# Performance work log

Measured on AMD Instinct MI355X. Metric: run time of the kernel, lower is better.

Reference implementation:

```python
import jax, jax.numpy as jnp
import numpy as np

TWO_PI = 2.0 * np.pi


def _unwrap(x):
    # torch: abs(x - 2*pi*round(x/(2*pi))) -> wrap to principal value, take magnitude
    return jnp.abs(x - TWO_PI * jnp.round(x / TWO_PI))


def _shift_diff_last(x):
    # Equivalent to matmul with M = triu(1,d=1)-triu(1,d=2)-eye (superdiag=+1, diag=-1):
    # out[..., 0] = -x[..., 0]; out[..., j] = x[..., j-1] - x[..., j]
    return jnp.concatenate([-x[..., :1], x[..., :-1] - x[..., 1:]], axis=-1)


def setup_inputs() -> dict:
    key = jax.random.key(0)
    k1, k2, k3, k4 = jax.random.split(key, 4)
    shape = (32, 1, 513, 512)  # [B, 1, nfreqs, frames]
    return {
        "spec_est_real": jax.random.normal(k1, shape, dtype=jnp.float32),
        "spec_est_imag": jax.random.normal(k2, shape, dtype=jnp.float32),
        "spec_ref_real": jax.random.normal(k3, shape, dtype=jnp.float32),
        "spec_ref_imag": jax.random.normal(k4, shape, dtype=jnp.float32),
    }


def reference(spec_est_real, spec_est_imag, spec_ref_real, spec_ref_imag):
    # torch.angle(complex).squeeze(1) -> [B, F, T]
    phase_g = jnp.arctan2(spec_est_imag, spec_est_real)[:, 0]
    phase_r = jnp.arctan2(spec_ref_imag, spec_ref_real)[:, 0]

    d = phase_r - phase_g  # [B, F, T]

    # IP loss
    ip_loss = jnp.mean(_unwrap(d))
    # GD: shift-difference along freq axis (GD_r - GD_g = shift_diff(phase_r - phase_g))
    gd_loss = jnp.mean(_unwrap(_shift_diff_last(jnp.swapaxes(d, 1, 2))))
    # PTD: shift-difference along time axis
    ptd_loss = jnp.mean(_unwrap(_shift_diff_last(d)))

    return ip_loss + gd_loss + ptd_loss
```

## Files before the change

kernel.cpp:

```cpp
#include <hip/hip_runtime.h>
#include <math.h>


#define NB 32
#define NF 513
#define NT 512
#define RPW 8
#define CHUNKS 65
#define NBLOCKS 520
#define NTOT 8404992LL

static __device__ __forceinline__ float fast_atan2(float y, float x) {
    const float PI_F  = 3.14159274101257324f;
    const float PI_2F = 1.57079632679489662f;
    float ax = fabsf(x), ay = fabsf(y);
    float mx = fmaxf(ax, ay), mn = fminf(ax, ay);
    float r  = mn * __builtin_amdgcn_rcpf(mx);
    r = (mx == 0.f) ? 0.f : r;
    float s = r * r;
    float p = fmaf(s, -0.01172120f, 0.05265332f);
    p = fmaf(s, p, -0.11643287f);
    p = fmaf(s, p,  0.19354346f);
    p = fmaf(s, p, -0.33262347f);
    p = fmaf(s, p,  0.99997726f);
    float a = r * p;
    a = (ay > ax) ? (PI_2F - a) : a;
    a = (x < 0.f) ? (PI_F - a) : a;
    return copysignf(a, y);
}

static __device__ __forceinline__ float pdiff(float a, float b, float c, float d) {
    return fast_atan2(fmaf(d, a, -(c * b)), fmaf(c, a, d * b));
}

static __device__ __forceinline__ float wrap_abs(float x) {
    const float PI_F     = 3.14159274101257324f;
    const float TWO_PI_F = 6.28318548202514648f;
    float u = fabsf(x);
    return u > PI_F ? TWO_PI_F - u : u;
}

struct Row8 { float4 a0, a1, b0, b1, c0, c1, e0, e1; };

static __device__ __forceinline__ void calc8(const Row8& r, float d[8]) {
    d[0] = pdiff(r.a0.x, r.b0.x, r.c0.x, r.e0.x);
    d[1] = pdiff(r.a0.y, r.b0.y, r.c0.y, r.e0.y);
    d[2] = pdiff(r.a0.z, r.b0.z, r.c0.z, r.e0.z);
    d[3] = pdiff(r.a0.w, r.b0.w, r.c0.w, r.e0.w);
    d[4] = pdiff(r.a1.x, r.b1.x, r.c1.x, r.e1.x);
    d[5] = pdiff(r.a1.y, r.b1.y, r.c1.y, r.e1.y);
    d[6] = pdiff(r.a1.z, r.b1.z, r.c1.z, r.e1.z);
    d[7] = pdiff(r.a1.w, r.b1.w, r.c1.w, r.e1.w);
}

__global__ __launch_bounds__(256) void phase_loss_k(
    const float* __restrict__ er, const float* __restrict__ ei,
    const float* __restrict__ rr, const float* __restrict__ ri,
    float* __restrict__ slots)
{
    const int tid  = threadIdx.x;
    const int lane = tid & 63;
    const int wid  = (blockIdx.x << 2) | (tid >> 6);
    const int b    = wid / CHUNKS;
    const int f0   = (wid - b * CHUNKS) * RPW;
    const int base = b * (NF * NT);

#define LOAD_ROW(dst, f_) do {                                   \
        const int _i = base + (f_) * NT + lane * 8;              \
        dst.a0 = *(const float4*)(er + _i);                      \
        dst.a1 = *(const float4*)(er + _i + 4);                  \
        dst.b0 = *(const float4*)(ei + _i);                      \
        dst.b1 = *(const float4*)(ei + _i + 4);                  \
        dst.c0 = *(const float4*)(rr + _i);                      \
        dst.c1 = *(const float4*)(rr + _i + 4);                  \
        dst.e0 = *(const float4*)(ri + _i);                      \
        dst.e1 = *(const float4*)(ri + _i + 4);                  \
    } while (0)

    float s = 0.f;
    float dp[8];
    Row8 cur, nxt;

    if (f0 > 0) LOAD_ROW(cur, f0 - 1);
    LOAD_ROW(nxt, f0);
    if (f0 > 0) {
        calc8(cur, dp);
    } else {
        #pragma unroll
        for (int k = 0; k < 8; ++k) dp[k] = 0.f;
    }

    #pragma unroll
    for (int r = 0; r < RPW; ++r) {
        const int f = f0 + r;
        if (f >= NF) break;
        cur = nxt;
        if (r + 1 < RPW && f + 1 < NF) LOAD_ROW(nxt, f + 1);
        float d[8];
        calc8(cur, d);
        float dt = __shfl_up(d[7], 1, 64);
        if (lane == 0) dt = 0.f;
        #pragma unroll
        for (int k = 0; k < 8; ++k) {
            s += fabsf(d[k]);
            s += wrap_abs(dp[k] - d[k]);
            s += wrap_abs(dt - d[k]);
            dt = d[k];
            dp[k] = d[k];
        }
    }
#undef LOAD_ROW

    #pragma unroll
    for (int off = 32; off > 0; off >>= 1)
        s += __shfl_down(s, off, 64);
    __shared__ float ws4[4];
    if (lane == 0) ws4[tid >> 6] = s;
    __syncthreads();
    if (tid == 0) slots[blockIdx.x] = ws4[0] + ws4[1] + ws4[2] + ws4[3];
}

__global__ __launch_bounds__(256) void finalize_k(const float* __restrict__ slots,
                                                  float* __restrict__ out)
{
    int tid = threadIdx.x;
    float s = 0.f;
    for (int i = tid; i < NBLOCKS; i += 256) s += slots[i];
    #pragma unroll
    for (int off = 32; off > 0; off >>= 1)
        s += __shfl_down(s, off, 64);
    __shared__ float wsum[4];
    if ((tid & 63) == 0) wsum[tid >> 6] = s;
    __syncthreads();
    if (tid == 0) {
        double tot = (double)wsum[0] + (double)wsum[1] + (double)wsum[2] + (double)wsum[3];
        out[0] = (float)(tot / (double)NTOT);
    }
}

extern "C" void kernel_launch(void* const* d_in, const int* in_sizes, int n_in,
                              void* d_out, int out_size, void* d_ws, size_t ws_size,
                              hipStream_t stream) {
    const float* er = (const float*)d_in[0];
    const float* ei = (const float*)d_in[1];
    const float* rr = (const float*)d_in[2];
    const float* ri = (const float*)d_in[3];
    float* out   = (float*)d_out;
    float* slots = (float*)d_ws;

    phase_loss_k<<<NBLOCKS, 256, 0, stream>>>(er, ei, rr, ri, slots);
    finalize_k<<<1, 256, 0, stream>>>(slots, out);
}
```

Measured before the change: 33.90 us.

## Fuse final reduction via last-block atomic counter and halve rows per wave

The separate finalize kernel is replaced by a last-block-done pattern: each block writes its partial sum, fences, and increments an atomic counter, and the last block reduces all slots. Rows per wave drop from 8 to 4, doubling the grid to improve occupancy and latency hiding. In exchange, each wave re-reads its halo row more often, adding extra global traffic, and a memset of the counter is added to the stream.

```diff
diff --git a/kernel.cpp b/kernel.cpp
--- a/kernel.cpp
+++ b/kernel.cpp
@@ -5,9 +5,9 @@
 #define NB 32
 #define NF 513
 #define NT 512
-#define RPW 8
-#define CHUNKS 65
-#define NBLOCKS 520
+#define RPW 4
+#define CHUNKS 129
+#define NBLOCKS 1032
 #define NTOT 8404992LL
 
 static __device__ __forceinline__ float fast_atan2(float y, float x) {
@@ -56,7 +56,8 @@
 __global__ __launch_bounds__(256) void phase_loss_k(
     const float* __restrict__ er, const float* __restrict__ ei,
     const float* __restrict__ rr, const float* __restrict__ ri,
-    float* __restrict__ slots)
+    float* __restrict__ slots, unsigned* __restrict__ cnt,
+    float* __restrict__ out)
 {
     const int tid  = threadIdx.x;
     const int lane = tid & 63;
@@ -115,26 +116,31 @@
     for (int off = 32; off > 0; off >>= 1)
         s += __shfl_down(s, off, 64);
     __shared__ float ws4[4];
+    __shared__ unsigned last_flag;
     if (lane == 0) ws4[tid >> 6] = s;
     __syncthreads();
-    if (tid == 0) slots[blockIdx.x] = ws4[0] + ws4[1] + ws4[2] + ws4[3];
-}
+    if (tid == 0) {
+        slots[blockIdx.x] = ws4[0] + ws4[1] + ws4[2] + ws4[3];
+        __threadfence();
+        unsigned prev = atomicAdd(cnt, 1u);
+        last_flag = (prev == NBLOCKS - 1) ? 1u : 0u;
+    }
+    __syncthreads();
 
-__global__ __launch_bounds__(256) void finalize_k(const float* __restrict__ slots,
-                                                  float* __restrict__ out)
-{
-    int tid = threadIdx.x;
-    float s = 0.f;
-    for (int i = tid; i < NBLOCKS; i += 256) s += slots[i];
-    #pragma unroll
-    for (int off = 32; off > 0; off >>= 1)
-        s += __shfl_down(s, off, 64);
-    __shared__ float wsum[4];
-    if ((tid & 63) == 0) wsum[tid >> 6] = s;
-    __syncthreads();
-    if (tid == 0) {
-        double tot = (double)wsum[0] + (double)wsum[1] + (double)wsum[2] + (double)wsum[3];
-        out[0] = (float)(tot / (double)NTOT);
+    if (last_flag) {
+        __threadfence();
+        float t = 0.f;
+        for (int i = tid; i < NBLOCKS; i += 256) t += slots[i];
+        #pragma unroll
+        for (int off = 32; off > 0; off >>= 1)
+            t += __shfl_down(t, off, 64);
+        __shared__ float fs4[4];
+        if (lane == 0) fs4[tid >> 6] = t;
+        __syncthreads();
+        if (tid == 0) {
+            double tot = (double)fs4[0] + (double)fs4[1] + (double)fs4[2] + (double)fs4[3];
+            out[0] = (float)(tot / (double)NTOT);
+        }
     }
 }
 
@@ -147,7 +153,9 @@
     const float* ri = (const float*)d_in[3];
     float* out   = (float*)d_out;
     float* slots = (float*)d_ws;
+    unsigned* cnt = (unsigned*)((char*)d_ws + NBLOCKS * sizeof(float));
 
-    phase_loss_k<<<NBLOCKS, 256, 0, stream>>>(er, ei, rr, ri, slots);
-    finalize_k<<<1, 256, 0, stream>>>(slots, out);
+    hipMemsetAsync(cnt, 0, sizeof(unsigned), stream);
+
+    phase_loss_k<<<NBLOCKS, 256, 0, stream>>>(er, ei, rr, ri, slots, cnt, out);
 }
```

Measured after the change: 69.20 us. 2.04x slower.

## Stage rows through LDS via async global_load_lds double buffering

Applied to the files above, without the earlier changes.

Rows are now loaded with global_load_lds straight into a per-wave double-buffered LDS slab, using manual vmcnt waits to keep the next row's loads in flight while the current row is computed. The lane-to-column mapping changes from 8 contiguous columns per lane to two 4-column halves, so the time-difference shuffle now handles a seam between the halves. The aim is deeper memory-level parallelism with fewer registers than the old register double buffering. In exchange it uses 64KB of LDS per block, which limits occupancy, and it relies on fragile inline waitcnt assembly.

```diff
diff --git a/kernel.cpp b/kernel.cpp
--- a/kernel.cpp
+++ b/kernel.cpp
@@ -7,6 +7,7 @@
 #define NT 512
 #define RPW 8
 #define CHUNKS 65
+#define NWAVES 2080
 #define NBLOCKS 520
 #define NTOT 8404992LL
 
@@ -40,17 +41,11 @@
     return u > PI_F ? TWO_PI_F - u : u;
 }
 
-struct Row8 { float4 a0, a1, b0, b1, c0, c1, e0, e1; };
-
-static __device__ __forceinline__ void calc8(const Row8& r, float d[8]) {
-    d[0] = pdiff(r.a0.x, r.b0.x, r.c0.x, r.e0.x);
-    d[1] = pdiff(r.a0.y, r.b0.y, r.c0.y, r.e0.y);
-    d[2] = pdiff(r.a0.z, r.b0.z, r.c0.z, r.e0.z);
-    d[3] = pdiff(r.a0.w, r.b0.w, r.c0.w, r.e0.w);
-    d[4] = pdiff(r.a1.x, r.b1.x, r.c1.x, r.e1.x);
-    d[5] = pdiff(r.a1.y, r.b1.y, r.c1.y, r.e1.y);
-    d[6] = pdiff(r.a1.z, r.b1.z, r.c1.z, r.e1.z);
-    d[7] = pdiff(r.a1.w, r.b1.w, r.c1.w, r.e1.w);
+static __device__ __forceinline__ void gll16(const float* g, float* l) {
+    __builtin_amdgcn_global_load_lds(
+        (const __attribute__((address_space(1))) void*)g,
+        (__attribute__((address_space(3))) void*)l,
+        16, 0, 0);
 }
 
 __global__ __launch_bounds__(256) void phase_loss_k(
@@ -58,64 +53,107 @@
     const float* __restrict__ rr, const float* __restrict__ ri,
     float* __restrict__ slots)
 {
+    __shared__ float lds_arr[4 * 4096];
     const int tid  = threadIdx.x;
     const int lane = tid & 63;
-    const int wid  = (blockIdx.x << 2) | (tid >> 6);
+    const int wave = tid >> 6;
+    const int wid  = (blockIdx.x << 2) | wave;
     const int b    = wid / CHUNKS;
     const int f0   = (wid - b * CHUNKS) * RPW;
     const int base = b * (NF * NT);
+    const int nv   = (NF - f0 < RPW) ? (NF - f0) : RPW;
+    const int fstart = (f0 > 0) ? f0 - 1 : f0;
+    const int nrows  = nv + (f0 > 0 ? 1 : 0);
 
-#define LOAD_ROW(dst, f_) do {                                   \
-        const int _i = base + (f_) * NT + lane * 8;              \
-        dst.a0 = *(const float4*)(er + _i);                      \
-        dst.a1 = *(const float4*)(er + _i + 4);                  \
-        dst.b0 = *(const float4*)(ei + _i);                      \
-        dst.b1 = *(const float4*)(ei + _i + 4);                  \
-        dst.c0 = *(const float4*)(rr + _i);                      \
-        dst.c1 = *(const float4*)(rr + _i + 4);                  \
-        dst.e0 = *(const float4*)(ri + _i);                      \
-        dst.e1 = *(const float4*)(ri + _i + 4);                  \
+    float* slab = &lds_arr[wave * 4096];
+
+#define ISSUE_ROW(p_, f_) do {                                    \
+        float* _buf = slab + (p_) * 2048;                         \
+        const int _ro = base + (f_) * NT + lane * 4;              \
+        gll16(er + _ro,       _buf);                              \
+        gll16(er + _ro + 256, _buf + 256);                        \
+        gll16(ei + _ro,       _buf + 512);                        \
+        gll16(ei + _ro + 256, _buf + 768);                        \
+        gll16(rr + _ro,       _buf + 1024);                       \
+        gll16(rr + _ro + 256, _buf + 1280);                       \
+        gll16(ri + _ro,       _buf + 1536);                       \
+        gll16(ri + _ro + 256, _buf + 1792);                       \
     } while (0)
+
+    ISSUE_ROW(0, fstart);
+    if (nrows > 1) ISSUE_ROW(1, fstart + 1);
 
     float s = 0.f;
     float dp[8];
-    Row8 cur, nxt;
+    #pragma unroll
+    for (int k = 0; k < 8; ++k) dp[k] = 0.f;
 
-    if (f0 > 0) LOAD_ROW(cur, f0 - 1);
-    LOAD_ROW(nxt, f0);
-    if (f0 > 0) {
-        calc8(cur, dp);
-    } else {
-        #pragma unroll
-        for (int k = 0; k < 8; ++k) dp[k] = 0.f;
-    }
+    for (int i = 0; i < nrows; ++i) {
+        if (i + 1 < nrows) {
+            asm volatile("s_waitcnt vmcnt(8)" ::: "memory");
+        } else {
+            asm volatile("s_waitcnt vmcnt(0)" ::: "memory");
+        }
+        __builtin_amdgcn_sched_barrier(0);
 
-    #pragma unroll
-    for (int r = 0; r < RPW; ++r) {
-        const int f = f0 + r;
-        if (f >= NF) break;
-        cur = nxt;
-        if (r + 1 < RPW && f + 1 < NF) LOAD_ROW(nxt, f + 1);
+        const float* buf = slab + (i & 1) * 2048;
+        float4 va0 = *(const float4*)(buf + lane * 4);
+        float4 va1 = *(const float4*)(buf + 256  + lane * 4);
+        float4 vb0 = *(const float4*)(buf + 512  + lane * 4);
+        float4 vb1 = *(const float4*)(buf + 768  + lane * 4);
+        float4 vc0 = *(const float4*)(buf + 1024 + lane * 4);
+        float4 vc1 = *(const float4*)(buf + 1280 + lane * 4);
+        float4 ve0 = *(const float4*)(buf + 1536 + lane * 4);
+        float4 ve1 = *(const float4*)(buf + 1792 + lane * 4);
+
+        asm volatile("s_waitcnt lgkmcnt(0)" ::: "memory");
+        __builtin_amdgcn_sched_barrier(0);
+        if (i + 2 < nrows) ISSUE_ROW(i & 1, fstart + i + 2);
+        __builtin_amdgcn_sched_barrier(0);
+
         float d[8];
-        calc8(cur, d);
-        float dt = __shfl_up(d[7], 1, 64);
-        if (lane == 0) dt = 0.f;
-        #pragma unroll
-        for (int k = 0; k < 8; ++k) {
-            s += fabsf(d[k]);
-            s += wrap_abs(dp[k] - d[k]);
-            s += wrap_abs(dt - d[k]);
-            dt = d[k];
-            dp[k] = d[k];
+        d[0] = pdiff(va0.x, vb0.x, vc0.x, ve0.x);
+        d[1] = pdiff(va0.y, vb0.y, vc0.y, ve0.y);
+        d[2] = pdiff(va0.z, vb0.z, vc0.z, ve0.z);
+        d[3] = pdiff(va0.w, vb0.w, vc0.w, ve0.w);
+        d[4] = pdiff(va1.x, vb1.x, vc1.x, ve1.x);
+        d[5] = pdiff(va1.y, vb1.y, vc1.y, ve1.y);
+        d[6] = pdiff(va1.z, vb1.z, vc1.z, ve1.z);
+        d[7] = pdiff(va1.w, vb1.w, vc1.w, ve1.w);
+
+        if (i == 0 && f0 > 0) {
+            #pragma unroll
+            for (int k = 0; k < 8; ++k) dp[k] = d[k];
+        } else {
+            float t255 = __shfl(d[3], 63, 64);
+            float dt0  = __shfl_up(d[3], 1, 64);
+            float dt1  = __shfl_up(d[7], 1, 64);
+            if (lane == 0) { dt0 = 0.f; dt1 = t255; }
+            #pragma unroll
+            for (int k = 0; k < 4; ++k) {
+                s += fabsf(d[k]);
+                s += wrap_abs(dp[k] - d[k]);
+                s += wrap_abs(dt0 - d[k]);
+                dt0 = d[k];
+                dp[k] = d[k];
+            }
+            #pragma unroll
+            for (int k = 4; k < 8; ++k) {
+                s += fabsf(d[k]);
+                s += wrap_abs(dp[k] - d[k]);
+                s += wrap_abs(dt1 - d[k]);
+                dt1 = d[k];
+                dp[k] = d[k];
+            }
         }
     }
-#undef LOAD_ROW
+#undef ISSUE_ROW
 
     #pragma unroll
     for (int off = 32; off > 0; off >>= 1)
         s += __shfl_down(s, off, 64);
     __shared__ float ws4[4];
-    if (lane == 0) ws4[tid >> 6] = s;
+    if (lane == 0) ws4[wave] = s;
     __syncthreads();
     if (tid == 0) slots[blockIdx.x] = ws4[0] + ws4[1] + ws4[2] + ws4[3];
 }
```

Result: slower. 36.31 us (+7.1%).
